# Optimization experiments

Hardware: AMD Instinct MI355X
Metric: run time of the kernel (lower is better)

The kernel has to match this reference:

```python
import jax, jax.numpy as jnp
import numpy as np
from jax import lax
from jax.scipy.special import gammaln, logsumexp

BIG_NEG = -1e9


def _emission_log_probs(features, means, cov):
    # Diagonal Gaussian per class; the torch module stores cov as a (D,D) matrix
    # whose diagonal holds the (tied) variances (eye at init, torch.diag after fit),
    # and uses scale_tril = cov.sqrt() in a MultivariateNormal.
    var = jnp.diagonal(cov)                                  # (D,)
    D = features.shape[-1]
    x2 = (features ** 2) @ (1.0 / var)                       # (B,N)
    cross = features @ (means / var).T                       # (B,N,C)
    m2 = jnp.sum(means ** 2 / var, axis=-1)                  # (C,)
    quad = x2[..., None] - 2.0 * cross + m2                  # (B,N,C)
    logdet = jnp.sum(jnp.log(var))
    return -0.5 * (quad + logdet + D * jnp.log(2.0 * jnp.pi))


def _semi_markov_logZ(emission, lengths, trans, init, len_lp, K):
    # Semi-Markov CRF forward DP (partition function).
    # alpha[t,c] = logsumexp_{k=1..K, valid} beta[t-k,c] + span_emit(t-k,t,c) + len_lp[k-1,c]
    # beta[s,c]  = logsumexp_src alpha[s,src] + trans[c,src]   (beta[0,:] = init)
    B, N, C = emission.shape
    CE = jnp.concatenate([jnp.zeros((B, 1, C), emission.dtype), jnp.cumsum(emission, axis=1)], axis=1)  # (B,N+1,C)
    CEpad = jnp.concatenate([jnp.zeros((B, K, C), emission.dtype), CE], axis=1)  # (B,N+1+K,C)
    betapad = jnp.full((B, N + 1 + K, C), BIG_NEG, emission.dtype)
    betapad = betapad.at[:, K, :].set(jnp.broadcast_to(init, (B, C)))
    len_rev = len_lp[::-1]  # window slot j corresponds to span length K - j

    def step(bp, t):
        idx = t + K
        bw = lax.dynamic_slice(bp, (0, idx - K, 0), (B, K, C))       # beta[t-K..t-1]
        cew = lax.dynamic_slice(CEpad, (0, idx - K, 0), (B, K, C))   # cumsum at span starts
        ce_t = lax.dynamic_slice(CEpad, (0, idx, 0), (B, 1, C))      # cumsum at t
        span = ce_t - cew                                            # (B,K,C) span emission sums
        alpha_t = logsumexp(bw + span + len_rev[None], axis=1)       # (B,C)
        beta_t = logsumexp(alpha_t[:, None, :] + trans[None, :, :], axis=2)  # (B, tgt)
        bp = lax.dynamic_update_slice(bp, beta_t[:, None, :], (0, idx, 0))
        return bp, alpha_t

    _, alphas = lax.scan(step, betapad, jnp.arange(1, N + 1))
    alphas = jnp.transpose(alphas, (1, 0, 2))                        # (B,N,C)
    idx = (lengths - 1).astype(jnp.int32)[:, None, None]
    alpha_T = jnp.take_along_axis(alphas, jnp.broadcast_to(idx, (B, 1, C)), axis=1)[:, 0, :]
    return logsumexp(alpha_T, axis=-1)                               # (B,) log partition


def setup_inputs() -> dict:
    key = jax.random.key(0)
    ks = jax.random.split(key, 6)
    B, N, C, D, K = 32, 1024, 64, 512, 20
    features = jax.random.normal(ks[0], (B, N, D), jnp.float32)
    lengths = jnp.full((B,), N, dtype=jnp.int32)
    gaussian_means = 0.1 * jax.random.normal(ks[1], (C, D), jnp.float32)
    gaussian_cov = jnp.eye(D, dtype=jnp.float32)
    transition_logits = 0.1 * jax.random.normal(ks[2], (C, C), jnp.float32)
    init_logits = jax.random.uniform(ks[3], (C,), jnp.float32)
    poisson_log_rates = jnp.log(5.0) + 0.1 * jax.random.normal(ks[4], (C,), jnp.float32)
    return {"features": features, "lengths": lengths, "gaussian_means": gaussian_means,
            "gaussian_cov": gaussian_cov, "transition_logits": transition_logits,
            "init_logits": init_logits, "poisson_log_rates": poisson_log_rates, "max_k": K}


def reference(features, lengths, gaussian_means, gaussian_cov, transition_logits,
              init_logits, poisson_log_rates, max_k):
    C = gaussian_means.shape[0]
    emission = _emission_log_probs(features, gaussian_means, gaussian_cov)      # (B,N,C)
    # no self transitions: mask diagonal, column-normalize (trans[tgt,src] = log p(tgt|src))
    masked = jnp.where(jnp.eye(C, dtype=bool), BIG_NEG, transition_logits)
    trans = jax.nn.log_softmax(masked, axis=0)
    init = jax.nn.log_softmax(init_logits)
    kvals = jnp.arange(1, max_k + 1, dtype=features.dtype)
    len_lp = (kvals[:, None] * poisson_log_rates[None, :]
              - jnp.exp(poisson_log_rates)[None, :]
              - gammaln(kvals + 1.0)[:, None])                                  # (K,C) Poisson log-pmf
    return _semi_markov_logZ(emission, lengths, trans, init, len_lp, max_k)
```

## Files before the change

kernel.cpp:

```cpp
#include <hip/hip_runtime.h>
#include <math.h>

#define CC 64
#define KK 20
#define DCH 32
#define LOG2E 1.4426950408889634f
#define LN2   0.6931471805599453f
#define LN2PI 1.8378770664093453f
#define BIGN  -1.0e9f

#if __has_builtin(__builtin_amdgcn_exp2f)
#define EXP2(x) __builtin_amdgcn_exp2f(x)
#else
#define EXP2(x) exp2f(x)
#endif
#if __has_builtin(__builtin_amdgcn_logf)
#define LOG2(x) __builtin_amdgcn_logf(x)
#else
#define LOG2(x) log2f(x)
#endif

typedef float v2f __attribute__((ext_vector_type(2)));
typedef float v4f __attribute__((ext_vector_type(4)));

__device__ __forceinline__ v2f pk_fma(v2f a, v2f b, v2f c) {
  v2f d;
  asm("v_pk_fma_f32 %0, %1, %2, %3" : "=v"(d) : "v"(a), "v"(b), "v"(c));
  return d;
}

__device__ __forceinline__ float rlane(float v, int l) {
  return __int_as_float(__builtin_amdgcn_readlane(__float_as_int(v), l));
}

template <int Ctrl, int OldBits>
__device__ __forceinline__ float dpp_mov(float x) {
  return __int_as_float(__builtin_amdgcn_update_dpp(
      OldBits, __float_as_int(x), Ctrl, 0xf, 0xf, false));
}

__device__ __forceinline__ float wave_max64(float x) {
  constexpr int NI = (int)0xff800000;
  x = fmaxf(x, dpp_mov<0x111, NI>(x));
  x = fmaxf(x, dpp_mov<0x112, NI>(x));
  x = fmaxf(x, dpp_mov<0x114, NI>(x));
  x = fmaxf(x, dpp_mov<0x118, NI>(x));
  x = fmaxf(x, dpp_mov<0x142, NI>(x));
  x = fmaxf(x, dpp_mov<0x143, NI>(x));
  return __int_as_float(__builtin_amdgcn_readlane(__float_as_int(x), 63));
}

__device__ __forceinline__ float wave_sum64(float x) {
  x += dpp_mov<0x111, 0>(x);
  x += dpp_mov<0x112, 0>(x);
  x += dpp_mov<0x114, 0>(x);
  x += dpp_mov<0x118, 0>(x);
  x += dpp_mov<0x142, 0>(x);
  x += dpp_mov<0x143, 0>(x);
  return __int_as_float(__builtin_amdgcn_readlane(__float_as_int(x), 63));
}

__global__ void setup_kernel(const float* __restrict__ means,
                             const float* __restrict__ cov,
                             const float* __restrict__ tl,
                             const float* __restrict__ il,
                             const float* __restrict__ plr,
                             float* __restrict__ wmat,
                             float* __restrict__ invvar,
                             float* __restrict__ sinv,
                             float* __restrict__ q2,
                             float* __restrict__ P_T,
                             float* __restrict__ init2,
                             float* __restrict__ len2,
                             int D) {
  __shared__ float red[256];
  int tid = threadIdx.x;
  for (int d = tid; d < D; d += 256) {
    float v = 1.0f / cov[(size_t)d * D + d];
    invvar[d] = v;
    sinv[d] = sqrtf(v);
  }
  float lp_ = 0.f;
  for (int d = tid; d < D; d += 256) lp_ += logf(cov[(size_t)d * D + d]);
  red[tid] = lp_;
  __syncthreads();
  for (int s = 128; s > 0; s >>= 1) {
    if (tid < s) red[tid] += red[tid + s];
    __syncthreads();
  }
  float logdet = red[0];
  __syncthreads();
  {
    int c = tid & 63, q = tid >> 6;
    int dq = D / 4;
    float m2p = 0.f;
    for (int d = q * dq; d < (q + 1) * dq; ++d) {
      float mu = means[c * D + d];
      m2p = fmaf(mu * mu, invvar[d], m2p);
    }
    red[tid] = m2p;
  }
  __syncthreads();
  for (int i = tid; i < CC * D; i += 256) wmat[i] = means[i] * sinv[i % D];
  if (tid < CC) {
    int c = tid;
    float m2 = red[c] + red[c + 64] + red[c + 128] + red[c + 192];
    q2[c] = -0.5f * LOG2E * (m2 + logdet + (float)D * LN2PI);
    int j = c;
    float mx = -1e30f;
    for (int i2 = 0; i2 < CC; ++i2) {
      float v = (i2 == j) ? BIGN : tl[i2 * CC + j];
      mx = fmaxf(mx, v);
    }
    float s = 0.f;
    for (int i2 = 0; i2 < CC; ++i2) {
      float v = (i2 == j) ? BIGN : tl[i2 * CC + j];
      s += expf(v - mx);
    }
    float inv = 1.f / s;
    for (int i2 = 0; i2 < CC; ++i2) {
      float v = (i2 == j) ? BIGN : tl[i2 * CC + j];
      P_T[j * CC + i2] = expf(v - mx) * inv;
    }
    float mi = -1e30f;
    for (int i2 = 0; i2 < CC; ++i2) mi = fmaxf(mi, il[i2]);
    float si = 0.f;
    for (int i2 = 0; i2 < CC; ++i2) si += expf(il[i2] - mi);
    init2[c] = LOG2E * (il[c] - (mi + logf(si)));
  }
  for (int i = tid; i < KK * CC; i += 256) {
    int k = i / CC, c = i % CC;
    float lr = plr[c];
    float lp = (float)(k + 1) * lr - expf(lr) - lgammaf((float)(k + 2));
    len2[i] = LOG2E * lp;
  }
}

__global__ __launch_bounds__(256) void emission_kernel(
    const float* __restrict__ feat,
    const float* __restrict__ wmat,
    const float* __restrict__ sinv,
    const float* __restrict__ q2,
    float* __restrict__ emhat,
    float* __restrict__ kmax,
    int D) {
  __shared__ __align__(16) float xsT[DCH][68];
  __shared__ __align__(16) float wsT[DCH][68];
  __shared__ float q2s[CC];
  __shared__ float x2row[64];
  __shared__ float rmx[64][17];
  __shared__ float kapsh[64];
  int tid = threadIdx.x;
  size_t row0 = (size_t)blockIdx.x * 64;
  if (tid < CC) q2s[tid] = q2[tid];
  int lr_ = tid >> 2;
  int lq  = tid & 3;
  int lj  = lq * 8;
  int tx = tid & 15, ty = tid >> 4;
  int r0 = ty * 4, c0 = tx * 4;

  const float* fx = feat + (row0 + (size_t)lr_) * D + lj;
  const float* fw = wmat + (size_t)lr_ * D + lj;
  const float* fs = sinv + lj;

  float4 xa = *(const float4*)(fx);
  float4 xb = *(const float4*)(fx + 4);
  float4 wa = *(const float4*)(fw);
  float4 wb = *(const float4*)(fw + 4);
  float4 sa = *(const float4*)(fs);
  float4 sb = *(const float4*)(fs + 4);

  float acc[4][4] = {{0.f}};
  float x2p = 0.f;

  for (int d0 = 0; d0 < D; d0 += DCH) {
    __syncthreads();
    {
      float xs0 = xa.x * sa.x, xs1 = xa.y * sa.y, xs2 = xa.z * sa.z, xs3 = xa.w * sa.w;
      float xs4 = xb.x * sb.x, xs5 = xb.y * sb.y, xs6 = xb.z * sb.z, xs7 = xb.w * sb.w;
      xsT[lj + 0][lr_] = xs0; xsT[lj + 1][lr_] = xs1;
      xsT[lj + 2][lr_] = xs2; xsT[lj + 3][lr_] = xs3;
      xsT[lj + 4][lr_] = xs4; xsT[lj + 5][lr_] = xs5;
      xsT[lj + 6][lr_] = xs6; xsT[lj + 7][lr_] = xs7;
      wsT[lj + 0][lr_] = wa.x; wsT[lj + 1][lr_] = wa.y;
      wsT[lj + 2][lr_] = wa.z; wsT[lj + 3][lr_] = wa.w;
      wsT[lj + 4][lr_] = wb.x; wsT[lj + 5][lr_] = wb.y;
      wsT[lj + 6][lr_] = wb.z; wsT[lj + 7][lr_] = wb.w;
      x2p = fmaf(xs0, xs0, x2p); x2p = fmaf(xs1, xs1, x2p);
      x2p = fmaf(xs2, xs2, x2p); x2p = fmaf(xs3, xs3, x2p);
      x2p = fmaf(xs4, xs4, x2p); x2p = fmaf(xs5, xs5, x2p);
      x2p = fmaf(xs6, xs6, x2p); x2p = fmaf(xs7, xs7, x2p);
    }
    __syncthreads();
    if (d0 + DCH < D) {
      fx += DCH; fw += DCH; fs += DCH;
      xa = *(const float4*)(fx);
      xb = *(const float4*)(fx + 4);
      wa = *(const float4*)(fw);
      wb = *(const float4*)(fw + 4);
      sa = *(const float4*)(fs);
      sb = *(const float4*)(fs + 4);
    }
    #pragma unroll
    for (int j = 0; j < DCH; ++j) {
      float4 xv = *(const float4*)&xsT[j][r0];
      float4 wv = *(const float4*)&wsT[j][c0];
      acc[0][0] = fmaf(xv.x, wv.x, acc[0][0]);
      acc[0][1] = fmaf(xv.x, wv.y, acc[0][1]);
      acc[0][2] = fmaf(xv.x, wv.z, acc[0][2]);
      acc[0][3] = fmaf(xv.x, wv.w, acc[0][3]);
      acc[1][0] = fmaf(xv.y, wv.x, acc[1][0]);
      acc[1][1] = fmaf(xv.y, wv.y, acc[1][1]);
      acc[1][2] = fmaf(xv.y, wv.z, acc[1][2]);
      acc[1][3] = fmaf(xv.y, wv.w, acc[1][3]);
      acc[2][0] = fmaf(xv.z, wv.x, acc[2][0]);
      acc[2][1] = fmaf(xv.z, wv.y, acc[2][1]);
      acc[2][2] = fmaf(xv.z, wv.z, acc[2][2]);
      acc[2][3] = fmaf(xv.z, wv.w, acc[2][3]);
      acc[3][0] = fmaf(xv.w, wv.x, acc[3][0]);
      acc[3][1] = fmaf(xv.w, wv.y, acc[3][1]);
      acc[3][2] = fmaf(xv.w, wv.z, acc[3][2]);
      acc[3][3] = fmaf(xv.w, wv.w, acc[3][3]);
    }
  }

  x2p += dpp_mov<0xB1, 0>(x2p);
  x2p += dpp_mov<0x4E, 0>(x2p);
  if (lq == 0) x2row[lr_] = x2p;
  __syncthreads();

  float e[4][4];
  #pragma unroll
  for (int i = 0; i < 4; ++i) {
    float h = 0.5f * x2row[r0 + i];
    #pragma unroll
    for (int k2 = 0; k2 < 4; ++k2)
      e[i][k2] = LOG2E * (acc[i][k2] - h) + q2s[c0 + k2];
  }
  #pragma unroll
  for (int i = 0; i < 4; ++i)
    rmx[r0 + i][tx] = fmaxf(fmaxf(e[i][0], e[i][1]), fmaxf(e[i][2], e[i][3]));
  __syncthreads();
  if (tid < 64) {
    float m = rmx[tid][0];
    #pragma unroll
    for (int j = 1; j < 16; ++j) m = fmaxf(m, rmx[tid][j]);
    kapsh[tid] = m;
    kmax[row0 + tid] = m;
  }
  __syncthreads();
  #pragma unroll
  for (int i = 0; i < 4; ++i) {
    float kp = kapsh[r0 + i];
    size_t row = row0 + r0 + i;
    float4 o;
    o.x = EXP2(e[i][0] - kp); o.y = EXP2(e[i][1] - kp);
    o.z = EXP2(e[i][2] - kp); o.w = EXP2(e[i][3] - kp);
    *(float4*)&emhat[row * CC + c0] = o;
  }
}

__global__ __launch_bounds__(64, 1) void recur_kernel(
    const float* __restrict__ emhat,
    const float* __restrict__ kmax,
    const float* __restrict__ P_T,
    const float* __restrict__ init2,
    const float* __restrict__ len2,
    const int* __restrict__ lengths,
    float* __restrict__ out,
    int N) {
  __shared__ __align__(16) float abuf[CC];
  int b = blockIdx.x;
  int c = threadIdx.x;

  v2f P2[CC / 2];
  #pragma unroll
  for (int j = 0; j < CC / 2; ++j) {
    v2f p;
    p.x = P_T[(size_t)(2 * j) * CC + c];
    p.y = P_T[(size_t)(2 * j + 1) * CC + c];
    P2[j] = p;
  }
  float W[KK + 1];
  #pragma unroll
  for (int k = 1; k <= KK; ++k) W[k] = EXP2(len2[(k - 1) * CC + c]);
  float W1 = W[1];

  const float* eh_b = emhat + (size_t)b * N * CC;
  const float* km_b = kmax + (size_t)b * N;
  int len_b = lengths[b];

  float skp = 0.f;
  for (int r = c; r < len_b; r += 64) skp += km_b[r];
  float Skap = wave_sum64(skp);

  float v = EXP2(init2[c]);
  float rho = eh_b[c];
  float q0v = eh_b[(size_t)(1 <= N - 1 ? 1 : N - 1) * CC + c];
  float q1v = eh_b[(size_t)(2 <= N - 1 ? 2 : N - 1) * CC + c];
  float q2v = eh_b[(size_t)(3 <= N - 1 ? 3 : N - 1) * CC + c];
  float q3v = eh_b[(size_t)(4 <= N - 1 ? 4 : N - 1) * CC + c];
  float EfSum = 0.f;
  float A[KK];
  #pragma unroll
  for (int i = 0; i < KK; ++i) A[i] = 0.f;
  float rest = 0.f;

  auto body = [&](int t, float& q) {
    float A0 = v * rho;
    float a = fmaf(A0, W1, rest);

    abuf[c] = a;
    v2f a2[CC / 2];
    #pragma unroll
    for (int j = 0; j < CC / 4; ++j) {
      v4f t4 = *(v4f*)&abuf[4 * j];
      v2f lo, hi;
      lo.x = t4.x; lo.y = t4.y;
      hi.x = t4.z; hi.y = t4.w;
      a2[2 * j] = lo;
      a2[2 * j + 1] = hi;
    }

    if (t == len_b) {
      float s_ = wave_sum64(a);
      if (c == 0) out[b] = LN2 * (Skap + EfSum + LOG2(s_));
    }

    float u0 = A0 * W[2], u1 = 0.f, u2 = 0.f, u3 = 0.f;
    #pragma unroll
    for (int i = 1; i + 3 <= 16; i += 4) {
      u0 = fmaf(A[i],     W[i + 2], u0);
      u1 = fmaf(A[i + 1], W[i + 3], u1);
      u2 = fmaf(A[i + 2], W[i + 4], u2);
      u3 = fmaf(A[i + 3], W[i + 5], u3);
    }
    u1 = fmaf(A[17], W[19], u1);
    u2 = fmaf(A[18], W[20], u2);
    float S2 = (u0 + u1) + (u2 + u3);

    float rh = q;
    int rown = (t + 4 <= N - 1) ? (t + 4) : (N - 1);
    q = eh_b[(size_t)rown * CC + c];

    float vmax = wave_max64(v);
    vmax = fminf(fmaxf(vmax, 1e-20f), 1e20f);
    int eb = (__float_as_int(vmax) >> 23) & 255;
    float scale = __int_as_float((254 - eb) << 23);
    EfSum += (float)(eb - 127);
    float rhon = rh * scale;
    rest = rhon * S2;

    #pragma unroll
    for (int i = KK - 1; i >= 2; --i) A[i] = A[i - 1] * rhon;
    A[1] = A0 * rhon;

    v2f m0 = {0.f, 0.f}, m1 = {0.f, 0.f}, m2 = {0.f, 0.f}, m3 = {0.f, 0.f};
    #pragma unroll
    for (int j = 0; j < CC / 2; j += 4) {
      m0 = pk_fma(P2[j],     a2[j],     m0);
      m1 = pk_fma(P2[j + 1], a2[j + 1], m1);
      m2 = pk_fma(P2[j + 2], a2[j + 2], m2);
      m3 = pk_fma(P2[j + 3], a2[j + 3], m3);
    }
    float vnew = ((m0.x + m0.y) + (m1.x + m1.y)) +
                 ((m2.x + m2.y) + (m3.x + m3.y));

    v = vnew;
    rho = rhon;
  };

  int t = 1;
  for (; t + 3 <= N; t += 4) {
    body(t,     q0v);
    body(t + 1, q1v);
    body(t + 2, q2v);
    body(t + 3, q3v);
  }
  for (; t <= N; ++t) {
    int s = t & 3;
    if (s == 1)      body(t, q0v);
    else if (s == 2) body(t, q1v);
    else if (s == 3) body(t, q2v);
    else             body(t, q3v);
  }
}

extern "C" void kernel_launch(void* const* d_in, const int* in_sizes, int n_in,
                              void* d_out, int out_size, void* d_ws, size_t ws_size,
                              hipStream_t stream) {
  const float* feat   = (const float*)d_in[0];
  const int*   lens   = (const int*)d_in[1];
  const float* means  = (const float*)d_in[2];
  const float* cov    = (const float*)d_in[3];
  const float* tl     = (const float*)d_in[4];
  const float* il     = (const float*)d_in[5];
  const float* plr    = (const float*)d_in[6];
  int B = in_sizes[1];
  int D = in_sizes[2] / CC;
  int N = in_sizes[0] / (B * D);

  float* ws = (float*)d_ws;
  size_t off = 0;
  float* wmat   = ws + off; off += (size_t)CC * D;
  float* invvar = ws + off; off += D;
  float* sinv   = ws + off; off += D;
  float* q2     = ws + off; off += CC;
  float* P_T    = ws + off; off += CC * CC;
  float* init2  = ws + off; off += CC;
  float* len2   = ws + off; off += KK * CC;
  float* emhat  = ws + off; off += (size_t)B * N * CC;
  float* kmax   = ws + off; off += (size_t)B * N;

  hipLaunchKernelGGL(setup_kernel, dim3(1), dim3(256), 0, stream,
                     means, cov, tl, il, plr, wmat, invvar, sinv, q2, P_T, init2, len2, D);
  hipLaunchKernelGGL(emission_kernel, dim3((B * N) / 64), dim3(256), 0, stream,
                     feat, wmat, sinv, q2, emhat, kmax, D);
  hipLaunchKernelGGL(recur_kernel, dim3(B), dim3(64), 0, stream,
                     emhat, kmax, P_T, init2, len2, lens, (float*)d_out, N);
}
```

Before: 516.9 us.

## Fuse two DP timesteps per body, sharing one renormalization and precomputing history dot products

Replaces the per-timestep body with a two-step body. It computes the length-window history dot products for both steps from the same A array before the recurrence chain, does the max-based rescaling only once per pair, and shifts the A history by two positions per pair. The aim is to take the independent dot-product work and the wave-wide max reduction off the serial dependency chain between steps. In exchange the code grows, register pressure rises, and the second step skips renormalization, which slightly raises the risk of overflow or underflow.

Measured after the change: 465.3 us. 1.11x faster.

```diff
diff --git a/kernel.cpp b/kernel.cpp
--- a/kernel.cpp
+++ b/kernel.cpp
@@ -27,10 +27,6 @@
   v2f d;
   asm("v_pk_fma_f32 %0, %1, %2, %3" : "=v"(d) : "v"(a), "v"(b), "v"(c));
   return d;
-}
-
-__device__ __forceinline__ float rlane(float v, int l) {
-  return __int_as_float(__builtin_amdgcn_readlane(__float_as_int(v), l));
 }
 
 template <int Ctrl, int OldBits>
@@ -306,10 +302,7 @@
   for (int i = 0; i < KK; ++i) A[i] = 0.f;
   float rest = 0.f;
 
-  auto body = [&](int t, float& q) {
-    float A0 = v * rho;
-    float a = fmaf(A0, W1, rest);
-
+  auto matvec = [&](float a) -> float {
     abuf[c] = a;
     v2f a2[CC / 2];
     #pragma unroll
@@ -321,28 +314,158 @@
       a2[2 * j] = lo;
       a2[2 * j + 1] = hi;
     }
-
+    v2f m0 = {0.f, 0.f}, m1 = {0.f, 0.f}, m2 = {0.f, 0.f}, m3 = {0.f, 0.f};
+    #pragma unroll
+    for (int j = 0; j < CC / 2; j += 4) {
+      m0 = pk_fma(P2[j],     a2[j],     m0);
+      m1 = pk_fma(P2[j + 1], a2[j + 1], m1);
+      m2 = pk_fma(P2[j + 2], a2[j + 2], m2);
+      m3 = pk_fma(P2[j + 3], a2[j + 3], m3);
+    }
+    return ((m0.x + m0.y) + (m1.x + m1.y)) + ((m2.x + m2.y) + (m3.x + m3.y));
+  };
+
+  auto body2 = [&](int t, float& qA, float& qB) {
+    float A0a = v * rho;
+    float aa = fmaf(A0a, W1, rest);
+
+    abuf[c] = aa;
+    v2f a2[CC / 2];
+    #pragma unroll
+    for (int j = 0; j < CC / 4; ++j) {
+      v4f t4 = *(v4f*)&abuf[4 * j];
+      v2f lo, hi;
+      lo.x = t4.x; lo.y = t4.y;
+      hi.x = t4.z; hi.y = t4.w;
+      a2[2 * j] = lo;
+      a2[2 * j + 1] = hi;
+    }
+
+    if (t == len_b) {
+      float s_ = wave_sum64(aa);
+      if (c == 0) out[b] = LN2 * (Skap + EfSum + LOG2(s_));
+    }
+
+    float d10 = 0.f, d11 = 0.f, d12 = 0.f, d13 = 0.f;
+    #pragma unroll
+    for (int i = 1; i + 3 <= 16; i += 4) {
+      d10 = fmaf(A[i],     W[i + 2], d10);
+      d11 = fmaf(A[i + 1], W[i + 3], d11);
+      d12 = fmaf(A[i + 2], W[i + 4], d12);
+      d13 = fmaf(A[i + 3], W[i + 5], d13);
+    }
+    d10 = fmaf(A[17], W[19], d10);
+    d11 = fmaf(A[18], W[20], d11);
+    float D1 = (d10 + d11) + (d12 + d13);
+
+    float vmax = wave_max64(v);
+    vmax = fminf(fmaxf(vmax, 1e-20f), 1e20f);
+    int eb = (__float_as_int(vmax) >> 23) & 255;
+    float scale = __int_as_float((254 - eb) << 23);
+    EfSum += (float)(eb - 127);
+
+    float rha = qA;
+    int rowa = (t + 4 <= N - 1) ? (t + 4) : (N - 1);
+    qA = eh_b[(size_t)rowa * CC + c];
+    float rhon_a = rha * scale;
+
+    float S2a = fmaf(A0a, W[2], D1);
+    rest = rhon_a * S2a;
+
+    {
+      v2f m0 = {0.f, 0.f}, m1 = {0.f, 0.f}, m2 = {0.f, 0.f}, m3 = {0.f, 0.f};
+      #pragma unroll
+      for (int j = 0; j < CC / 2; j += 4) {
+        m0 = pk_fma(P2[j],     a2[j],     m0);
+        m1 = pk_fma(P2[j + 1], a2[j + 1], m1);
+        m2 = pk_fma(P2[j + 2], a2[j + 2], m2);
+        m3 = pk_fma(P2[j + 3], a2[j + 3], m3);
+      }
+      v = ((m0.x + m0.y) + (m1.x + m1.y)) + ((m2.x + m2.y) + (m3.x + m3.y));
+    }
+
+    float A0b = v * rhon_a;
+    float ab = fmaf(A0b, W1, rest);
+
+    abuf[c] = ab;
+    v2f b2[CC / 2];
+    #pragma unroll
+    for (int j = 0; j < CC / 4; ++j) {
+      v4f t4 = *(v4f*)&abuf[4 * j];
+      v2f lo, hi;
+      lo.x = t4.x; lo.y = t4.y;
+      hi.x = t4.z; hi.y = t4.w;
+      b2[2 * j] = lo;
+      b2[2 * j + 1] = hi;
+    }
+
+    if (t + 1 == len_b) {
+      float s_ = wave_sum64(ab);
+      if (c == 0) out[b] = LN2 * (Skap + EfSum + LOG2(s_));
+    }
+
+    float d20 = 0.f, d21 = 0.f, d22 = 0.f, d23 = 0.f;
+    #pragma unroll
+    for (int i = 1; i + 3 <= 16; i += 4) {
+      d20 = fmaf(A[i],     W[i + 3], d20);
+      d21 = fmaf(A[i + 1], W[i + 4], d21);
+      d22 = fmaf(A[i + 2], W[i + 5], d22);
+      d23 = fmaf(A[i + 3], W[i + 6], d23);
+    }
+    d20 = fmaf(A[17], W[20], d20);
+    float D2 = (d20 + d21) + (d22 + d23);
+
+    float rhb = qB;
+    int rowb = (t + 5 <= N - 1) ? (t + 5) : (N - 1);
+    qB = eh_b[(size_t)rowb * CC + c];
+    float rhon_b = rhb;
+
+    float S2b = fmaf(A0b, W[2], rhon_a * fmaf(A0a, W[3], D2));
+    rest = rhon_b * S2b;
+
+    float r2 = rhon_a * rhon_b;
+    #pragma unroll
+    for (int i = 18; i >= 3; --i) A[i] = A[i - 2] * r2;
+    A[2] = A0a * r2;
+    A[1] = A0b * rhon_b;
+
+    {
+      v2f m0 = {0.f, 0.f}, m1 = {0.f, 0.f}, m2 = {0.f, 0.f}, m3 = {0.f, 0.f};
+      #pragma unroll
+      for (int j = 0; j < CC / 2; j += 4) {
+        m0 = pk_fma(P2[j],     b2[j],     m0);
+        m1 = pk_fma(P2[j + 1], b2[j + 1], m1);
+        m2 = pk_fma(P2[j + 2], b2[j + 2], m2);
+        m3 = pk_fma(P2[j + 3], b2[j + 3], m3);
+      }
+      v = ((m0.x + m0.y) + (m1.x + m1.y)) + ((m2.x + m2.y) + (m3.x + m3.y));
+    }
+
+    rho = rhon_b;
+  };
+
+  auto body1 = [&](int t, float& q) {
+    float A0 = v * rho;
+    float a = fmaf(A0, W1, rest);
+    float vn = matvec(a);
     if (t == len_b) {
       float s_ = wave_sum64(a);
       if (c == 0) out[b] = LN2 * (Skap + EfSum + LOG2(s_));
     }
-
-    float u0 = A0 * W[2], u1 = 0.f, u2 = 0.f, u3 = 0.f;
+    float d10 = A0 * W[2], d11 = 0.f, d12 = 0.f, d13 = 0.f;
     #pragma unroll
     for (int i = 1; i + 3 <= 16; i += 4) {
-      u0 = fmaf(A[i],     W[i + 2], u0);
-      u1 = fmaf(A[i + 1], W[i + 3], u1);
-      u2 = fmaf(A[i + 2], W[i + 4], u2);
-      u3 = fmaf(A[i + 3], W[i + 5], u3);
-    }
-    u1 = fmaf(A[17], W[19], u1);
-    u2 = fmaf(A[18], W[20], u2);
-    float S2 = (u0 + u1) + (u2 + u3);
-
+      d10 = fmaf(A[i],     W[i + 2], d10);
+      d11 = fmaf(A[i + 1], W[i + 3], d11);
+      d12 = fmaf(A[i + 2], W[i + 4], d12);
+      d13 = fmaf(A[i + 3], W[i + 5], d13);
+    }
+    d11 = fmaf(A[17], W[19], d11);
+    d12 = fmaf(A[18], W[20], d12);
+    float S2 = (d10 + d11) + (d12 + d13);
     float rh = q;
     int rown = (t + 4 <= N - 1) ? (t + 4) : (N - 1);
     q = eh_b[(size_t)rown * CC + c];
-
     float vmax = wave_max64(v);
     vmax = fminf(fmaxf(vmax, 1e-20f), 1e20f);
     int eb = (__float_as_int(vmax) >> 23) & 255;
@@ -350,39 +473,24 @@
     EfSum += (float)(eb - 127);
     float rhon = rh * scale;
     rest = rhon * S2;
-
-    #pragma unroll
-    for (int i = KK - 1; i >= 2; --i) A[i] = A[i - 1] * rhon;
+    #pragma unroll
+    for (int i = 18; i >= 2; --i) A[i] = A[i - 1] * rhon;
     A[1] = A0 * rhon;
-
-    v2f m0 = {0.f, 0.f}, m1 = {0.f, 0.f}, m2 = {0.f, 0.f}, m3 = {0.f, 0.f};
-    #pragma unroll
-    for (int j = 0; j < CC / 2; j += 4) {
-      m0 = pk_fma(P2[j],     a2[j],     m0);
-      m1 = pk_fma(P2[j + 1], a2[j + 1], m1);
-      m2 = pk_fma(P2[j + 2], a2[j + 2], m2);
-      m3 = pk_fma(P2[j + 3], a2[j + 3], m3);
-    }
-    float vnew = ((m0.x + m0.y) + (m1.x + m1.y)) +
-                 ((m2.x + m2.y) + (m3.x + m3.y));
-
-    v = vnew;
+    v = vn;
     rho = rhon;
   };
 
   int t = 1;
   for (; t + 3 <= N; t += 4) {
-    body(t,     q0v);
-    body(t + 1, q1v);
-    body(t + 2, q2v);
-    body(t + 3, q3v);
+    body2(t,     q0v, q1v);
+    body2(t + 2, q2v, q3v);
   }
   for (; t <= N; ++t) {
     int s = t & 3;
-    if (s == 1)      body(t, q0v);
-    else if (s == 2) body(t, q1v);
-    else if (s == 3) body(t, q2v);
-    else             body(t, q3v);
+    if (s == 1)      body1(t, q0v);
+    else if (s == 2) body1(t, q1v);
+    else if (s == 3) body1(t, q2v);
+    else             body1(t, q3v);
   }
 }
 
```

## Block the semi-Markov recurrence four steps at a time and double-buffer emission LDS

Applied to the files above, without the earlier changes.

The forward DP loop now advances four time steps per iteration. The span-history dot products for all four steps are computed up front from the old A window, and the newly produced A0 terms are folded in through nested FMAs. The window shift then happens once per four steps, using a combined rescale product. Renormalisation is done once per block instead of every step, and this takes the scalar work off the serial dependency chain. The emission GEMM also gets double-buffered shared-memory tiles, which removes one barrier per chunk, at the cost of more LDS and some reordering of floating-point accumulation.

New measurement: 447.4 us. -13.4%, faster.

```diff
diff --git a/kernel.cpp b/kernel.cpp
--- a/kernel.cpp
+++ b/kernel.cpp
@@ -27,10 +27,6 @@
   v2f d;
   asm("v_pk_fma_f32 %0, %1, %2, %3" : "=v"(d) : "v"(a), "v"(b), "v"(c));
   return d;
-}
-
-__device__ __forceinline__ float rlane(float v, int l) {
-  return __int_as_float(__builtin_amdgcn_readlane(__float_as_int(v), l));
 }
 
 template <int Ctrl, int OldBits>
@@ -144,8 +140,8 @@
     float* __restrict__ emhat,
     float* __restrict__ kmax,
     int D) {
-  __shared__ __align__(16) float xsT[DCH][68];
-  __shared__ __align__(16) float wsT[DCH][68];
+  __shared__ __align__(16) float xsT[2][DCH][68];
+  __shared__ __align__(16) float wsT[2][DCH][68];
   __shared__ float q2s[CC];
   __shared__ float x2row[64];
   __shared__ float rmx[64][17];
@@ -173,38 +169,38 @@
   float acc[4][4] = {{0.f}};
   float x2p = 0.f;
 
+  {
+    float xs0 = xa.x * sa.x, xs1 = xa.y * sa.y, xs2 = xa.z * sa.z, xs3 = xa.w * sa.w;
+    float xs4 = xb.x * sb.x, xs5 = xb.y * sb.y, xs6 = xb.z * sb.z, xs7 = xb.w * sb.w;
+    xsT[0][lj + 0][lr_] = xs0; xsT[0][lj + 1][lr_] = xs1;
+    xsT[0][lj + 2][lr_] = xs2; xsT[0][lj + 3][lr_] = xs3;
+    xsT[0][lj + 4][lr_] = xs4; xsT[0][lj + 5][lr_] = xs5;
+    xsT[0][lj + 6][lr_] = xs6; xsT[0][lj + 7][lr_] = xs7;
+    wsT[0][lj + 0][lr_] = wa.x; wsT[0][lj + 1][lr_] = wa.y;
+    wsT[0][lj + 2][lr_] = wa.z; wsT[0][lj + 3][lr_] = wa.w;
+    wsT[0][lj + 4][lr_] = wb.x; wsT[0][lj + 5][lr_] = wb.y;
+    wsT[0][lj + 6][lr_] = wb.z; wsT[0][lj + 7][lr_] = wb.w;
+    x2p = fmaf(xs0, xs0, x2p); x2p = fmaf(xs1, xs1, x2p);
+    x2p = fmaf(xs2, xs2, x2p); x2p = fmaf(xs3, xs3, x2p);
+    x2p = fmaf(xs4, xs4, x2p); x2p = fmaf(xs5, xs5, x2p);
+    x2p = fmaf(xs6, xs6, x2p); x2p = fmaf(xs7, xs7, x2p);
+  }
+  int cur = 0;
   for (int d0 = 0; d0 < D; d0 += DCH) {
     __syncthreads();
-    {
-      float xs0 = xa.x * sa.x, xs1 = xa.y * sa.y, xs2 = xa.z * sa.z, xs3 = xa.w * sa.w;
-      float xs4 = xb.x * sb.x, xs5 = xb.y * sb.y, xs6 = xb.z * sb.z, xs7 = xb.w * sb.w;
-      xsT[lj + 0][lr_] = xs0; xsT[lj + 1][lr_] = xs1;
-      xsT[lj + 2][lr_] = xs2; xsT[lj + 3][lr_] = xs3;
-      xsT[lj + 4][lr_] = xs4; xsT[lj + 5][lr_] = xs5;
-      xsT[lj + 6][lr_] = xs6; xsT[lj + 7][lr_] = xs7;
-      wsT[lj + 0][lr_] = wa.x; wsT[lj + 1][lr_] = wa.y;
-      wsT[lj + 2][lr_] = wa.z; wsT[lj + 3][lr_] = wa.w;
-      wsT[lj + 4][lr_] = wb.x; wsT[lj + 5][lr_] = wb.y;
-      wsT[lj + 6][lr_] = wb.z; wsT[lj + 7][lr_] = wb.w;
-      x2p = fmaf(xs0, xs0, x2p); x2p = fmaf(xs1, xs1, x2p);
-      x2p = fmaf(xs2, xs2, x2p); x2p = fmaf(xs3, xs3, x2p);
-      x2p = fmaf(xs4, xs4, x2p); x2p = fmaf(xs5, xs5, x2p);
-      x2p = fmaf(xs6, xs6, x2p); x2p = fmaf(xs7, xs7, x2p);
-    }
-    __syncthreads();
-    if (d0 + DCH < D) {
-      fx += DCH; fw += DCH; fs += DCH;
-      xa = *(const float4*)(fx);
-      xb = *(const float4*)(fx + 4);
-      wa = *(const float4*)(fw);
-      wb = *(const float4*)(fw + 4);
-      sa = *(const float4*)(fs);
-      sb = *(const float4*)(fs + 4);
+    bool more = (d0 + DCH) < D;
+    if (more) {
+      xa = *(const float4*)(fx + d0 + DCH);
+      xb = *(const float4*)(fx + d0 + DCH + 4);
+      wa = *(const float4*)(fw + d0 + DCH);
+      wb = *(const float4*)(fw + d0 + DCH + 4);
+      sa = *(const float4*)(fs + d0 + DCH);
+      sb = *(const float4*)(fs + d0 + DCH + 4);
     }
     #pragma unroll
     for (int j = 0; j < DCH; ++j) {
-      float4 xv = *(const float4*)&xsT[j][r0];
-      float4 wv = *(const float4*)&wsT[j][c0];
+      float4 xv = *(const float4*)&xsT[cur][j][r0];
+      float4 wv = *(const float4*)&wsT[cur][j][c0];
       acc[0][0] = fmaf(xv.x, wv.x, acc[0][0]);
       acc[0][1] = fmaf(xv.x, wv.y, acc[0][1]);
       acc[0][2] = fmaf(xv.x, wv.z, acc[0][2]);
@@ -222,6 +218,24 @@
       acc[3][2] = fmaf(xv.w, wv.z, acc[3][2]);
       acc[3][3] = fmaf(xv.w, wv.w, acc[3][3]);
     }
+    if (more) {
+      int nxt = cur ^ 1;
+      float xs0 = xa.x * sa.x, xs1 = xa.y * sa.y, xs2 = xa.z * sa.z, xs3 = xa.w * sa.w;
+      float xs4 = xb.x * sb.x, xs5 = xb.y * sb.y, xs6 = xb.z * sb.z, xs7 = xb.w * sb.w;
+      xsT[nxt][lj + 0][lr_] = xs0; xsT[nxt][lj + 1][lr_] = xs1;
+      xsT[nxt][lj + 2][lr_] = xs2; xsT[nxt][lj + 3][lr_] = xs3;
+      xsT[nxt][lj + 4][lr_] = xs4; xsT[nxt][lj + 5][lr_] = xs5;
+      xsT[nxt][lj + 6][lr_] = xs6; xsT[nxt][lj + 7][lr_] = xs7;
+      wsT[nxt][lj + 0][lr_] = wa.x; wsT[nxt][lj + 1][lr_] = wa.y;
+      wsT[nxt][lj + 2][lr_] = wa.z; wsT[nxt][lj + 3][lr_] = wa.w;
+      wsT[nxt][lj + 4][lr_] = wb.x; wsT[nxt][lj + 5][lr_] = wb.y;
+      wsT[nxt][lj + 6][lr_] = wb.z; wsT[nxt][lj + 7][lr_] = wb.w;
+      x2p = fmaf(xs0, xs0, x2p); x2p = fmaf(xs1, xs1, x2p);
+      x2p = fmaf(xs2, xs2, x2p); x2p = fmaf(xs3, xs3, x2p);
+      x2p = fmaf(xs4, xs4, x2p); x2p = fmaf(xs5, xs5, x2p);
+      x2p = fmaf(xs6, xs6, x2p); x2p = fmaf(xs7, xs7, x2p);
+    }
+    cur ^= 1;
   }
 
   x2p += dpp_mov<0xB1, 0>(x2p);
@@ -296,53 +310,157 @@
 
   float v = EXP2(init2[c]);
   float rho = eh_b[c];
-  float q0v = eh_b[(size_t)(1 <= N - 1 ? 1 : N - 1) * CC + c];
-  float q1v = eh_b[(size_t)(2 <= N - 1 ? 2 : N - 1) * CC + c];
-  float q2v = eh_b[(size_t)(3 <= N - 1 ? 3 : N - 1) * CC + c];
-  float q3v = eh_b[(size_t)(4 <= N - 1 ? 4 : N - 1) * CC + c];
+  float qa = eh_b[(size_t)(1 <= N - 1 ? 1 : N - 1) * CC + c];
+  float qb = eh_b[(size_t)(2 <= N - 1 ? 2 : N - 1) * CC + c];
+  float qc = eh_b[(size_t)(3 <= N - 1 ? 3 : N - 1) * CC + c];
+  float qd = eh_b[(size_t)(4 <= N - 1 ? 4 : N - 1) * CC + c];
   float EfSum = 0.f;
   float A[KK];
   #pragma unroll
   for (int i = 0; i < KK; ++i) A[i] = 0.f;
   float rest = 0.f;
 
-  auto body = [&](int t, float& q) {
-    float A0 = v * rho;
-    float a = fmaf(A0, W1, rest);
-
+  auto bcast = [&](float a, v2f* dst) {
     abuf[c] = a;
-    v2f a2[CC / 2];
     #pragma unroll
     for (int j = 0; j < CC / 4; ++j) {
       v4f t4 = *(v4f*)&abuf[4 * j];
       v2f lo, hi;
       lo.x = t4.x; lo.y = t4.y;
       hi.x = t4.z; hi.y = t4.w;
-      a2[2 * j] = lo;
-      a2[2 * j + 1] = hi;
-    }
-
+      dst[2 * j] = lo;
+      dst[2 * j + 1] = hi;
+    }
+  };
+  auto consume = [&](const v2f* a2) -> float {
+    v2f m0 = {0.f, 0.f}, m1 = {0.f, 0.f}, m2 = {0.f, 0.f}, m3 = {0.f, 0.f};
+    #pragma unroll
+    for (int j = 0; j < CC / 2; j += 4) {
+      m0 = pk_fma(P2[j],     a2[j],     m0);
+      m1 = pk_fma(P2[j + 1], a2[j + 1], m1);
+      m2 = pk_fma(P2[j + 2], a2[j + 2], m2);
+      m3 = pk_fma(P2[j + 3], a2[j + 3], m3);
+    }
+    return ((m0.x + m0.y) + (m1.x + m1.y)) + ((m2.x + m2.y) + (m3.x + m3.y));
+  };
+
+  auto body4 = [&](int t, float& qa_, float& qb_, float& qc_, float& qd_) {
+    v2f a2[CC / 2];
+    float A0a = v * rho;
+    float aa = fmaf(A0a, W1, rest);
+    bcast(aa, a2);
+    if (t == len_b) {
+      float s_ = wave_sum64(aa);
+      if (c == 0) out[b] = LN2 * (Skap + EfSum + LOG2(s_));
+    }
+    float D1 = 0.f, D2 = 0.f, D3 = 0.f, D4 = 0.f;
+    #pragma unroll
+    for (int i = 1; i <= 15; ++i) {
+      float ai = A[i];
+      D1 = fmaf(ai, W[i + 2], D1);
+      D2 = fmaf(ai, W[i + 3], D2);
+      D3 = fmaf(ai, W[i + 4], D3);
+      D4 = fmaf(ai, W[i + 5], D4);
+    }
+    D1 = fmaf(A[16], W[18], D1); D2 = fmaf(A[16], W[19], D2); D3 = fmaf(A[16], W[20], D3);
+    D1 = fmaf(A[17], W[19], D1); D2 = fmaf(A[17], W[20], D2);
+    D1 = fmaf(A[18], W[20], D1);
+    float vmax = wave_max64(v);
+    vmax = fminf(fmaxf(vmax, 1e-20f), 1e20f);
+    int eb = (__float_as_int(vmax) >> 23) & 255;
+    float scale = __int_as_float((254 - eb) << 23);
+    EfSum += (float)(eb - 127);
+    float ra = qa_ * scale;
+    {
+      int rr = (t + 4 <= N - 1) ? (t + 4) : (N - 1);
+      qa_ = eh_b[(size_t)rr * CC + c];
+    }
+    rest = ra * fmaf(A0a, W[2], D1);
+    v = consume(a2);
+
+    float A0b = v * ra;
+    float ab = fmaf(A0b, W1, rest);
+    bcast(ab, a2);
+    if (t + 1 == len_b) {
+      float s_ = wave_sum64(ab);
+      if (c == 0) out[b] = LN2 * (Skap + EfSum + LOG2(s_));
+    }
+    float rb = qb_;
+    {
+      int rr = (t + 5 <= N - 1) ? (t + 5) : (N - 1);
+      qb_ = eh_b[(size_t)rr * CC + c];
+    }
+    rest = rb * fmaf(A0b, W[2], ra * fmaf(A0a, W[3], D2));
+    v = consume(a2);
+
+    float A0c = v * rb;
+    float ac = fmaf(A0c, W1, rest);
+    bcast(ac, a2);
+    if (t + 2 == len_b) {
+      float s_ = wave_sum64(ac);
+      if (c == 0) out[b] = LN2 * (Skap + EfSum + LOG2(s_));
+    }
+    float rc = qc_;
+    {
+      int rr = (t + 6 <= N - 1) ? (t + 6) : (N - 1);
+      qc_ = eh_b[(size_t)rr * CC + c];
+    }
+    rest = rc * fmaf(A0c, W[2], rb * fmaf(A0b, W[3], ra * fmaf(A0a, W[4], D3)));
+    v = consume(a2);
+
+    float A0d = v * rc;
+    float ad = fmaf(A0d, W1, rest);
+    bcast(ad, a2);
+    if (t + 3 == len_b) {
+      float s_ = wave_sum64(ad);
+      if (c == 0) out[b] = LN2 * (Skap + EfSum + LOG2(s_));
+    }
+    float rd = qd_;
+    {
+      int rr = (t + 7 <= N - 1) ? (t + 7) : (N - 1);
+      qd_ = eh_b[(size_t)rr * CC + c];
+    }
+    rest = rd * fmaf(A0d, W[2],
+                rc * fmaf(A0c, W[3],
+                rb * fmaf(A0b, W[4],
+                ra * fmaf(A0a, W[5], D4))));
+    float rcd = rc * rd;
+    float rbcd = rb * rcd;
+    float r4 = ra * rbcd;
+    #pragma unroll
+    for (int i = 18; i >= 5; --i) A[i] = A[i - 4] * r4;
+    A[4] = A0a * r4;
+    A[3] = A0b * rbcd;
+    A[2] = A0c * rcd;
+    A[1] = A0d * rd;
+    v = consume(a2);
+
+    rho = rd;
+  };
+
+  auto body1 = [&](int t, float& q) {
+    v2f a2[CC / 2];
+    float A0 = v * rho;
+    float a = fmaf(A0, W1, rest);
+    bcast(a, a2);
     if (t == len_b) {
       float s_ = wave_sum64(a);
       if (c == 0) out[b] = LN2 * (Skap + EfSum + LOG2(s_));
     }
-
-    float u0 = A0 * W[2], u1 = 0.f, u2 = 0.f, u3 = 0.f;
+    float d10 = A0 * W[2], d11 = 0.f, d12 = 0.f, d13 = 0.f;
     #pragma unroll
     for (int i = 1; i + 3 <= 16; i += 4) {
-      u0 = fmaf(A[i],     W[i + 2], u0);
-      u1 = fmaf(A[i + 1], W[i + 3], u1);
-      u2 = fmaf(A[i + 2], W[i + 4], u2);
-      u3 = fmaf(A[i + 3], W[i + 5], u3);
-    }
-    u1 = fmaf(A[17], W[19], u1);
-    u2 = fmaf(A[18], W[20], u2);
-    float S2 = (u0 + u1) + (u2 + u3);
-
+      d10 = fmaf(A[i],     W[i + 2], d10);
+      d11 = fmaf(A[i + 1], W[i + 3], d11);
+      d12 = fmaf(A[i + 2], W[i + 4], d12);
+      d13 = fmaf(A[i + 3], W[i + 5], d13);
+    }
+    d11 = fmaf(A[17], W[19], d11);
+    d12 = fmaf(A[18], W[20], d12);
+    float S2 = (d10 + d11) + (d12 + d13);
     float rh = q;
     int rown = (t + 4 <= N - 1) ? (t + 4) : (N - 1);
     q = eh_b[(size_t)rown * CC + c];
-
     float vmax = wave_max64(v);
     vmax = fminf(fmaxf(vmax, 1e-20f), 1e20f);
     int eb = (__float_as_int(vmax) >> 23) & 255;
@@ -350,39 +468,21 @@
     EfSum += (float)(eb - 127);
     float rhon = rh * scale;
     rest = rhon * S2;
-
-    #pragma unroll
-    for (int i = KK - 1; i >= 2; --i) A[i] = A[i - 1] * rhon;
+    #pragma unroll
+    for (int i = 18; i >= 2; --i) A[i] = A[i - 1] * rhon;
     A[1] = A0 * rhon;
-
-    v2f m0 = {0.f, 0.f}, m1 = {0.f, 0.f}, m2 = {0.f, 0.f}, m3 = {0.f, 0.f};
-    #pragma unroll
-    for (int j = 0; j < CC / 2; j += 4) {
-      m0 = pk_fma(P2[j],     a2[j],     m0);
-      m1 = pk_fma(P2[j + 1], a2[j + 1], m1);
-      m2 = pk_fma(P2[j + 2], a2[j + 2], m2);
-      m3 = pk_fma(P2[j + 3], a2[j + 3], m3);
-    }
-    float vnew = ((m0.x + m0.y) + (m1.x + m1.y)) +
-                 ((m2.x + m2.y) + (m3.x + m3.y));
-
-    v = vnew;
+    v = consume(a2);
     rho = rhon;
   };
 
   int t = 1;
-  for (; t + 3 <= N; t += 4) {
-    body(t,     q0v);
-    body(t + 1, q1v);
-    body(t + 2, q2v);
-    body(t + 3, q3v);
-  }
+  for (; t + 3 <= N; t += 4) body4(t, qa, qb, qc, qd);
   for (; t <= N; ++t) {
     int s = t & 3;
-    if (s == 1)      body(t, q0v);
-    else if (s == 2) body(t, q1v);
-    else if (s == 3) body(t, q2v);
-    else             body(t, q3v);
+    if (s == 1)      body1(t, qa);
+    else if (s == 2) body1(t, qb);
+    else if (s == 3) body1(t, qc);
+    else             body1(t, qd);
   }
 }
 
```

## Block the semi-Markov recurrence four steps at a time with packed window updates

Applied to the files above, without the earlier changes.

Reworks the per-step recurrence so that four time steps share one pass over the duration window. The window sums for all four steps are computed up front with packed FMAs, and the window array is shifted by four slots at once using a combined scale factor. The old code shifted and rescaled the full window every step, and this change is meant to remove most of that serial scalar work from the critical path. The cost is more register pressure, a per-step scale that is now applied differently across the block, and a scalar tail loop that handles the last steps.

After: 420.7 us. 1.23x faster.

```diff
diff --git a/kernel.cpp b/kernel.cpp
--- a/kernel.cpp
+++ b/kernel.cpp
@@ -27,10 +27,6 @@
   v2f d;
   asm("v_pk_fma_f32 %0, %1, %2, %3" : "=v"(d) : "v"(a), "v"(b), "v"(c));
   return d;
-}
-
-__device__ __forceinline__ float rlane(float v, int l) {
-  return __int_as_float(__builtin_amdgcn_readlane(__float_as_int(v), l));
 }
 
 template <int Ctrl, int OldBits>
@@ -260,6 +256,8 @@
   }
 }
 
+#define AE(i) (A2[((i) - 1) >> 1][((i) - 1) & 1])
+
 __global__ __launch_bounds__(64, 1) void recur_kernel(
     const float* __restrict__ emhat,
     const float* __restrict__ kmax,
@@ -281,10 +279,14 @@
     p.y = P_T[(size_t)(2 * j + 1) * CC + c];
     P2[j] = p;
   }
-  float W[KK + 1];
-  #pragma unroll
-  for (int k = 1; k <= KK; ++k) W[k] = EXP2(len2[(k - 1) * CC + c]);
-  float W1 = W[1];
+  float Wl[KK + 1];
+  #pragma unroll
+  for (int k = 1; k <= KK; ++k) Wl[k] = EXP2(len2[(k - 1) * CC + c]);
+  float W1 = Wl[1], w2 = Wl[2], w3 = Wl[3], w4 = Wl[4], w5 = Wl[5];
+  v2f Wq[21];
+  #pragma unroll
+  for (int m = 3; m <= 19; ++m) { Wq[m].x = Wl[m]; Wq[m].y = Wl[m + 1]; }
+  Wq[20].x = Wl[20]; Wq[20].y = 0.f;
 
   const float* eh_b = emhat + (size_t)b * N * CC;
   const float* km_b = kmax + (size_t)b * N;
@@ -296,53 +298,144 @@
 
   float v = EXP2(init2[c]);
   float rho = eh_b[c];
-  float q0v = eh_b[(size_t)(1 <= N - 1 ? 1 : N - 1) * CC + c];
-  float q1v = eh_b[(size_t)(2 <= N - 1 ? 2 : N - 1) * CC + c];
-  float q2v = eh_b[(size_t)(3 <= N - 1 ? 3 : N - 1) * CC + c];
-  float q3v = eh_b[(size_t)(4 <= N - 1 ? 4 : N - 1) * CC + c];
+  float qa = eh_b[(size_t)(1 <= N - 1 ? 1 : N - 1) * CC + c];
+  float qb = eh_b[(size_t)(2 <= N - 1 ? 2 : N - 1) * CC + c];
+  float qc = eh_b[(size_t)(3 <= N - 1 ? 3 : N - 1) * CC + c];
+  float qd = eh_b[(size_t)(4 <= N - 1 ? 4 : N - 1) * CC + c];
   float EfSum = 0.f;
-  float A[KK];
-  #pragma unroll
-  for (int i = 0; i < KK; ++i) A[i] = 0.f;
+  v2f A2[10];
+  #pragma unroll
+  for (int j = 0; j < 10; ++j) { A2[j].x = 0.f; A2[j].y = 0.f; }
   float rest = 0.f;
 
-  auto body = [&](int t, float& q) {
-    float A0 = v * rho;
-    float a = fmaf(A0, W1, rest);
-
+  const float* pa = eh_b + (size_t)5 * CC + c;
+  const float* pb = pa + CC;
+  const float* pc = pb + CC;
+  const float* pd = pc + CC;
+
+  auto bcast = [&](float a, v2f* dst) {
     abuf[c] = a;
-    v2f a2[CC / 2];
     #pragma unroll
     for (int j = 0; j < CC / 4; ++j) {
       v4f t4 = *(v4f*)&abuf[4 * j];
       v2f lo, hi;
       lo.x = t4.x; lo.y = t4.y;
       hi.x = t4.z; hi.y = t4.w;
-      a2[2 * j] = lo;
-      a2[2 * j + 1] = hi;
-    }
-
+      dst[2 * j] = lo;
+      dst[2 * j + 1] = hi;
+    }
+  };
+  auto consume = [&](const v2f* a2) -> float {
+    v2f m0 = {0.f, 0.f}, m1 = {0.f, 0.f}, m2 = {0.f, 0.f}, m3 = {0.f, 0.f};
+    #pragma unroll
+    for (int j = 0; j < CC / 2; j += 4) {
+      m0 = pk_fma(P2[j],     a2[j],     m0);
+      m1 = pk_fma(P2[j + 1], a2[j + 1], m1);
+      m2 = pk_fma(P2[j + 2], a2[j + 2], m2);
+      m3 = pk_fma(P2[j + 3], a2[j + 3], m3);
+    }
+    v2f s0 = m0 + m1;
+    v2f s1 = m2 + m3;
+    v2f s = s0 + s1;
+    return s.x + s.y;
+  };
+
+  auto body4 = [&](int t) {
+    v2f a2[CC / 2];
+    float A0a = v * rho;
+    float aa = fmaf(A0a, W1, rest);
+    bcast(aa, a2);
+    if (t == len_b) {
+      float s_ = wave_sum64(aa);
+      if (c == 0) out[b] = LN2 * (Skap + EfSum + LOG2(s_));
+    }
+    v2f d1 = {0.f, 0.f}, d2 = {0.f, 0.f}, d3 = {0.f, 0.f}, d4 = {0.f, 0.f};
+    #pragma unroll
+    for (int j = 0; j <= 8; ++j) d1 = pk_fma(A2[j], Wq[2 * j + 3], d1);
+    #pragma unroll
+    for (int j = 0; j <= 8; ++j) d2 = pk_fma(A2[j], Wq[2 * j + 4], d2);
+    #pragma unroll
+    for (int j = 0; j <= 7; ++j) d3 = pk_fma(A2[j], Wq[2 * j + 5], d3);
+    #pragma unroll
+    for (int j = 0; j <= 7; ++j) d4 = pk_fma(A2[j], Wq[2 * j + 6], d4);
+    float D1 = d1.x + d1.y, D2 = d2.x + d2.y;
+    float D3 = d3.x + d3.y, D4 = d4.x + d4.y;
+    float vmax = wave_max64(v);
+    vmax = fminf(fmaxf(vmax, 1e-20f), 1e20f);
+    int eb = (__float_as_int(vmax) >> 23) & 255;
+    float scale = __int_as_float((254 - eb) << 23);
+    EfSum += (float)(eb - 127);
+    float ra = qa * scale;
+    qa = *pa; pa += 4 * CC;
+    rest = ra * fmaf(A0a, w2, D1);
+    v = consume(a2);
+
+    float A0b = v * ra;
+    float ab = fmaf(A0b, W1, rest);
+    bcast(ab, a2);
+    if (t + 1 == len_b) {
+      float s_ = wave_sum64(ab);
+      if (c == 0) out[b] = LN2 * (Skap + EfSum + LOG2(s_));
+    }
+    float rb = qb;
+    qb = *pb; pb += 4 * CC;
+    rest = rb * fmaf(A0b, w2, ra * fmaf(A0a, w3, D2));
+    v = consume(a2);
+
+    float A0c = v * rb;
+    float ac = fmaf(A0c, W1, rest);
+    bcast(ac, a2);
+    if (t + 2 == len_b) {
+      float s_ = wave_sum64(ac);
+      if (c == 0) out[b] = LN2 * (Skap + EfSum + LOG2(s_));
+    }
+    float rc = qc;
+    qc = *pc; pc += 4 * CC;
+    rest = rc * fmaf(A0c, w2, rb * fmaf(A0b, w3, ra * fmaf(A0a, w4, D3)));
+    v = consume(a2);
+
+    float A0d = v * rc;
+    float ad = fmaf(A0d, W1, rest);
+    bcast(ad, a2);
+    if (t + 3 == len_b) {
+      float s_ = wave_sum64(ad);
+      if (c == 0) out[b] = LN2 * (Skap + EfSum + LOG2(s_));
+    }
+    float rd = qd;
+    qd = *pd; pd += 4 * CC;
+    rest = rd * fmaf(A0d, w2,
+                rc * fmaf(A0c, w3,
+                rb * fmaf(A0b, w4,
+                ra * fmaf(A0a, w5, D4))));
+    float rcd = rc * rd;
+    float rbcd = rb * rcd;
+    float r4 = ra * rbcd;
+    v2f r4v; r4v.x = r4; r4v.y = r4;
+    #pragma unroll
+    for (int j = 9; j >= 2; --j) A2[j] = A2[j - 2] * r4v;
+    A2[1].x = A0b * rbcd; A2[1].y = A0a * r4;
+    A2[0].x = A0d * rd;   A2[0].y = A0c * rcd;
+    v = consume(a2);
+
+    rho = rd;
+  };
+
+  auto body1 = [&](int t, float& q) {
+    v2f a2[CC / 2];
+    float A0 = v * rho;
+    float a = fmaf(A0, W1, rest);
+    bcast(a, a2);
     if (t == len_b) {
       float s_ = wave_sum64(a);
       if (c == 0) out[b] = LN2 * (Skap + EfSum + LOG2(s_));
     }
-
-    float u0 = A0 * W[2], u1 = 0.f, u2 = 0.f, u3 = 0.f;
-    #pragma unroll
-    for (int i = 1; i + 3 <= 16; i += 4) {
-      u0 = fmaf(A[i],     W[i + 2], u0);
-      u1 = fmaf(A[i + 1], W[i + 3], u1);
-      u2 = fmaf(A[i + 2], W[i + 4], u2);
-      u3 = fmaf(A[i + 3], W[i + 5], u3);
-    }
-    u1 = fmaf(A[17], W[19], u1);
-    u2 = fmaf(A[18], W[20], u2);
-    float S2 = (u0 + u1) + (u2 + u3);
-
+    v2f d1 = {0.f, 0.f};
+    #pragma unroll
+    for (int j = 0; j <= 8; ++j) d1 = pk_fma(A2[j], Wq[2 * j + 3], d1);
+    float S2 = fmaf(A0, w2, d1.x + d1.y);
     float rh = q;
     int rown = (t + 4 <= N - 1) ? (t + 4) : (N - 1);
     q = eh_b[(size_t)rown * CC + c];
-
     float vmax = wave_max64(v);
     vmax = fminf(fmaxf(vmax, 1e-20f), 1e20f);
     int eb = (__float_as_int(vmax) >> 23) & 255;
@@ -350,39 +443,21 @@
     EfSum += (float)(eb - 127);
     float rhon = rh * scale;
     rest = rhon * S2;
-
-    #pragma unroll
-    for (int i = KK - 1; i >= 2; --i) A[i] = A[i - 1] * rhon;
-    A[1] = A0 * rhon;
-
-    v2f m0 = {0.f, 0.f}, m1 = {0.f, 0.f}, m2 = {0.f, 0.f}, m3 = {0.f, 0.f};
-    #pragma unroll
-    for (int j = 0; j < CC / 2; j += 4) {
-      m0 = pk_fma(P2[j],     a2[j],     m0);
-      m1 = pk_fma(P2[j + 1], a2[j + 1], m1);
-      m2 = pk_fma(P2[j + 2], a2[j + 2], m2);
-      m3 = pk_fma(P2[j + 3], a2[j + 3], m3);
-    }
-    float vnew = ((m0.x + m0.y) + (m1.x + m1.y)) +
-                 ((m2.x + m2.y) + (m3.x + m3.y));
-
-    v = vnew;
+    #pragma unroll
+    for (int i = 20; i >= 2; --i) AE(i) = AE(i - 1) * rhon;
+    AE(1) = A0 * rhon;
+    v = consume(a2);
     rho = rhon;
   };
 
   int t = 1;
-  for (; t + 3 <= N; t += 4) {
-    body(t,     q0v);
-    body(t + 1, q1v);
-    body(t + 2, q2v);
-    body(t + 3, q3v);
-  }
+  for (; t <= N - 8; t += 4) body4(t);
   for (; t <= N; ++t) {
     int s = t & 3;
-    if (s == 1)      body(t, q0v);
-    else if (s == 2) body(t, q1v);
-    else if (s == 3) body(t, q2v);
-    else             body(t, q3v);
+    if (s == 1)      body1(t, qa);
+    else if (s == 2) body1(t, qb);
+    else if (s == 3) body1(t, qc);
+    else             body1(t, qd);
   }
 }
 
```
